# Kernel tuning notes

Hardware: AMD Instinct MI355X
Metric: run time of the kernel (lower is better)

## Reference

```python
import jax, jax.numpy as jnp
import numpy as np

B, S, E = 2, 2048, 5120
HQ, HKV, HD = 32, 8, 128          # q heads, kv heads, head_dim (hard-coded 128 in source)
DQ, DKV = HQ * HD, HKV * HD       # 4096, 1024
ROPE_THETA = 1.0e9
NEG = -1e30


def setup_inputs() -> dict:
    key = jax.random.key(0)
    k0, k1, k2, k3, k4 = jax.random.split(key, 5)
    x = jax.random.normal(k0, (B, S, E), jnp.float32)
    wq = jax.random.normal(k1, (DQ, E), jnp.float32) * 0.02
    wk = jax.random.normal(k2, (DKV, E), jnp.float32) * 0.02
    wv = jax.random.normal(k3, (DKV, E), jnp.float32) * 0.02
    wo = jax.random.normal(k4, (E, DQ), jnp.float32) * 0.02
    # rotary frequencies: complex freqs_cis[s, HD//2] = exp(i * s * theta^{-2j/HD})
    inv_freq = 1.0 / (ROPE_THETA ** (jnp.arange(0, HD, 2, dtype=jnp.float32) / HD))  # [64]
    ang = jnp.arange(S, dtype=jnp.float32)[:, None] * inv_freq[None, :]              # [S, 64]
    return {
        "x": x,
        "freqs_cos": jnp.cos(ang),
        "freqs_sin": jnp.sin(ang),
        "wq": wq, "wk": wk, "wv": wv, "wo": wo,
    }


def _apply_rope(t, cos, sin):
    # t: [b, s, h, HD//2, 2] viewed as complex pairs; cos/sin: [1, s, 1, HD//2]
    tr, ti = t[..., 0], t[..., 1]
    out = jnp.stack([tr * cos - ti * sin, tr * sin + ti * cos], axis=-1)
    b, s, h = t.shape[0], t.shape[1], t.shape[2]
    return out.reshape(b, s, h, HD)


def reference(x, freqs_cos, freqs_sin, wq, wk, wv, wo):
    b, s, _ = x.shape
    q = (x @ wq.T).reshape(b, s, HQ, HD // 2, 2)
    k = (x @ wk.T).reshape(b, s, HKV, HD // 2, 2)
    v = (x @ wv.T).reshape(b, s, HKV, HD)
    cos = freqs_cos[:s][None, :, None, :]
    sin = freqs_sin[:s][None, :, None, :]
    q = _apply_rope(q, cos, sin)                       # [b, s, HQ, HD]
    k = _apply_rope(k, cos, sin)                       # [b, s, HKV, HD]
    # GQA repeat_kv (repeat_interleave along head dim)
    k = jnp.repeat(k, HQ // HKV, axis=2)               # [b, s, HQ, HD]
    v = jnp.repeat(v, HQ // HKV, axis=2)
    q = q.transpose(0, 2, 1, 3)                        # [b, HQ, s, HD]
    k = k.transpose(0, 2, 1, 3)
    v = v.transpose(0, 2, 1, 3)
    scale = 1.0 / np.sqrt(HD).astype(np.float32)
    scores = jnp.einsum('bhqd,bhkd->bhqk', q, k) * scale
    causal = jnp.tril(jnp.ones((s, s), dtype=bool))
    scores = jnp.where(causal[None, None], scores, NEG)
    attn = jax.nn.softmax(scores, axis=-1)
    out = jnp.einsum('bhqk,bhkd->bhqd', attn, v)       # [b, HQ, s, HD]
    out = out.transpose(0, 2, 1, 3).reshape(b, s, DQ)
    return out @ wo.T                                  # [b, s, E]
```

## Files before the change

kernel.cpp:

```cpp
#include <hip/hip_runtime.h>


typedef unsigned short u16;
typedef __bf16 bf16x8 __attribute__((ext_vector_type(8)));
typedef __bf16 bf16x4 __attribute__((ext_vector_type(4)));
typedef float f32x4 __attribute__((ext_vector_type(4)));

__device__ __forceinline__ u16 f2bf(float f) {
  unsigned u = __builtin_bit_cast(unsigned, f);
  u += 0x7fff + ((u >> 16) & 1);
  return (u16)(u >> 16);
}
__device__ __forceinline__ float bf2f(u16 h) {
  unsigned u = ((unsigned)h) << 16;
  return __builtin_bit_cast(float, u);
}

__device__ __forceinline__ float exp2_hw(float x) {
#if __has_builtin(__builtin_amdgcn_exp2f)
  return __builtin_amdgcn_exp2f(x);
#else
  return __expf(x * 0.6931471805599453f);
#endif
}

__device__ __forceinline__ void gload_lds16(const u16* g, u16* lds) {
  __builtin_amdgcn_global_load_lds(
      (const __attribute__((address_space(1))) void*)g,
      (__attribute__((address_space(3))) void*)lds, 16, 0, 0);
}

__device__ __forceinline__ f32x4 mfma16(bf16x8 a, bf16x8 b, f32x4 c) {
  return __builtin_amdgcn_mfma_f32_16x16x32_bf16(a, b, c, 0, 0, 0);
}

#define VMW(N) asm volatile("s_waitcnt vmcnt(" #N ")" ::: "memory")
#define BAR()  __builtin_amdgcn_s_barrier()

__global__ __launch_bounds__(256) void cvt_kernel(const float4* __restrict__ in,
                                                  uint2* __restrict__ out, int n4) {
  int i = blockIdx.x * blockDim.x + threadIdx.x;
  if (i >= n4) return;
  float4 v = in[i];
  unsigned lo = (unsigned)f2bf(v.x) | ((unsigned)f2bf(v.y) << 16);
  unsigned hi = (unsigned)f2bf(v.z) | ((unsigned)f2bf(v.w) << 16);
  out[i] = make_uint2(lo, hi);
}

__global__ __launch_bounds__(256) void rope_kernel(u16* __restrict__ t,
                                                   const float* __restrict__ fcos,
                                                   const float* __restrict__ fsin,
                                                   int hsh, float scale, int total) {
  int idx = blockIdx.x * blockDim.x + threadIdx.x;
  if (idx >= total) return;
  int j = idx & 63;
  int s = (idx >> (6 + hsh)) & 2047;
  float c = fcos[s * 64 + j], sn = fsin[s * 64 + j];
  unsigned* p = (unsigned*)(t + (size_t)idx * 2);
  unsigned v = *p;
  float tr = bf2f((u16)(v & 0xffffu)), ti = bf2f((u16)(v >> 16));
  float orr = (tr * c - ti * sn) * scale;
  float oi  = (tr * sn + ti * c) * scale;
  *p = (unsigned)f2bf(orr) | ((unsigned)f2bf(oi) << 16);
}

template <int MODE>
__global__ __launch_bounds__(256) void gemm_bt(const u16* __restrict__ A,
                                               const u16* __restrict__ B,
                                               void* __restrict__ Cout,
                                               int M, int N, int K) {
  __shared__ u16 As[8192];
  __shared__ u16 Bs[8192];
  const int tid = threadIdx.x;
  const int lane = tid & 63, wave = tid >> 6;
  const int wm = wave >> 1, wn = wave & 1;
  int gx = gridDim.x, nwg = gx * gridDim.y;
  int lin = blockIdx.y * gx + blockIdx.x;
  if ((nwg & 7) == 0) lin = (lin & 7) * (nwg >> 3) + (lin >> 3);
  const int m0 = (lin / gx) * 128, n0 = (lin % gx) * 128;
  const int lc = lane & 15, lg = lane >> 4;

  f32x4 acc[4][4] = {};
  const int sr = tid >> 3, sc = tid & 7;

  for (int kt = 0; kt < K; kt += 64) {
    __syncthreads();
#pragma unroll
    for (int q = 0; q < 4; ++q) {
      int r = q * 32 + sr;
      int cc = sc ^ (r & 7);
      gload_lds16(A + (size_t)(m0 + r) * K + kt + cc * 8, &As[q * 2048 + tid * 8]);
      gload_lds16(B + (size_t)(n0 + r) * K + kt + cc * 8, &Bs[q * 2048 + tid * 8]);
    }
    __syncthreads();
#pragma unroll
    for (int ks = 0; ks < 2; ++ks) {
      bf16x8 af[4], bfr[4];
#pragma unroll
      for (int m = 0; m < 4; ++m) {
        int r = wm * 64 + m * 16 + lc;
        int gc = ks * 4 + lg;
        af[m] = *(const bf16x8*)&As[r * 64 + ((gc ^ (r & 7)) * 8)];
      }
#pragma unroll
      for (int n = 0; n < 4; ++n) {
        int r = wn * 64 + n * 16 + lc;
        int gc = ks * 4 + lg;
        bfr[n] = *(const bf16x8*)&Bs[r * 64 + ((gc ^ (r & 7)) * 8)];
      }
#pragma unroll
      for (int m = 0; m < 4; ++m)
#pragma unroll
        for (int n = 0; n < 4; ++n)
          acc[m][n] = mfma16(af[m], bfr[n], acc[m][n]);
    }
  }

#pragma unroll
  for (int m = 0; m < 4; ++m) {
#pragma unroll
    for (int n = 0; n < 4; ++n) {
#pragma unroll
      for (int i = 0; i < 4; ++i) {
        int gm = m0 + wm * 64 + m * 16 + lg * 4 + i;
        int gn = n0 + wn * 64 + n * 16 + lc;
        float v = acc[m][n][i];
        if (MODE == 0) {
          ((u16*)Cout)[(size_t)gm * N + gn] = f2bf(v);
        } else {
          size_t addr = ((size_t)((gm >> 11) * 8 + (gn >> 7)) * 128 + (gn & 127)) * 2048 +
                        (gm & 2047);
          ((u16*)Cout)[addr] = f2bf(v);
        }
      }
    }
  }
}

template <int OUT_F32>
__global__ __launch_bounds__(512, 2) void gemm256(const u16* __restrict__ A,
                                                  const u16* __restrict__ B,
                                                  void* __restrict__ Cout,
                                                  int M, int N, int K) {
  __shared__ u16 lds[2][2][2][8192];
  const int tid = threadIdx.x, lane = tid & 63, wave = tid >> 6;
  const int wm = wave >> 2;
  const int wn = wave & 3;
  const int lc = lane & 15, lg = lane >> 4;
  const int srow = lane >> 3;
  const int cc8  = ((lane & 7) ^ srow) * 8;
  const int bh   = wn >> 1;
  const int sb   = wm * 2 + (wn & 1);

  int gx = gridDim.x, nwg = gx * gridDim.y;
  int lin = blockIdx.y * gx + blockIdx.x;
  if ((nwg & 7) == 0) lin = (lin & 7) * (nwg >> 3) + (lin >> 3);
  const int m0 = (lin / gx) * 256, n0 = (lin % gx) * 256;

  auto stA = [&](int buf, int kcol, int rowBase) {
    int rb = rowBase + wn * 8;
    gload_lds16(A + (size_t)(m0 + wm * 128 + rb + srow) * K + kcol + cc8,
                &lds[buf][0][wm][rb * 64 + lane * 8]);
  };
  auto stB = [&](int buf, int kcol, int rowBase) {
    int rb = rowBase + sb * 8;
    gload_lds16(B + (size_t)(n0 + bh * 128 + rb + srow) * K + kcol + cc8,
                &lds[buf][1][bh][rb * 64 + lane * 8]);
  };
  auto stageAll = [&](int buf, int kcol) {
    stA(buf, kcol, 0);  stB(buf, kcol, 0);
    stA(buf, kcol, 32); stB(buf, kcol, 32);
    stA(buf, kcol, 64); stB(buf, kcol, 64);
    stA(buf, kcol, 96); stB(buf, kcol, 96);
  };

  f32x4 acc[8][4] = {};
  bf16x8 af[4][2], bfv[4][2];

  stageAll(0, 0);

  const int nk = K >> 6;
  for (int t = 0; t < nk; ++t) {
    const int cur = t & 1;
    if (t + 1 < nk) {
      stageAll(cur ^ 1, (t + 1) << 6);
      VMW(8);
    } else {
      VMW(0);
    }
    BAR();
    const u16* Ah = &lds[cur][0][wm][0];
    const u16* Bh = &lds[cur][1][bh][0];

#pragma unroll
    for (int m = 0; m < 4; ++m)
#pragma unroll
      for (int kg = 0; kg < 2; ++kg) {
        int r = m * 16 + lc;
        af[m][kg] = *(const bf16x8*)&Ah[r * 64 + (((kg * 4 + lg) ^ (r & 7)) * 8)];
      }
#pragma unroll
    for (int n = 0; n < 2; ++n)
#pragma unroll
      for (int kg = 0; kg < 2; ++kg) {
        int r = (wn & 1) * 64 + n * 16 + lc;
        bfv[n][kg] = *(const bf16x8*)&Bh[r * 64 + (((kg * 4 + lg) ^ (r & 7)) * 8)];
      }
    __builtin_amdgcn_s_setprio(1);
#pragma unroll
    for (int m = 0; m < 4; ++m)
#pragma unroll
      for (int n = 0; n < 2; ++n)
#pragma unroll
        for (int kg = 0; kg < 2; ++kg)
          acc[m][n] = mfma16(af[m][kg], bfv[n][kg], acc[m][n]);
    __builtin_amdgcn_s_setprio(0);

#pragma unroll
    for (int n = 2; n < 4; ++n)
#pragma unroll
      for (int kg = 0; kg < 2; ++kg) {
        int r = (wn & 1) * 64 + n * 16 + lc;
        bfv[n][kg] = *(const bf16x8*)&Bh[r * 64 + (((kg * 4 + lg) ^ (r & 7)) * 8)];
      }
    __builtin_amdgcn_s_setprio(1);
#pragma unroll
    for (int m = 0; m < 4; ++m)
#pragma unroll
      for (int n = 2; n < 4; ++n)
#pragma unroll
        for (int kg = 0; kg < 2; ++kg)
          acc[m][n] = mfma16(af[m][kg], bfv[n][kg], acc[m][n]);
    __builtin_amdgcn_s_setprio(0);

#pragma unroll
    for (int m = 0; m < 4; ++m)
#pragma unroll
      for (int kg = 0; kg < 2; ++kg) {
        int r = 64 + m * 16 + lc;
        af[m][kg] = *(const bf16x8*)&Ah[r * 64 + (((kg * 4 + lg) ^ (r & 7)) * 8)];
      }
    __builtin_amdgcn_s_setprio(1);
#pragma unroll
    for (int m = 0; m < 4; ++m)
#pragma unroll
      for (int n = 0; n < 4; ++n)
#pragma unroll
        for (int kg = 0; kg < 2; ++kg)
          acc[4 + m][n] = mfma16(af[m][kg], bfv[n][kg], acc[4 + m][n]);
    __builtin_amdgcn_s_setprio(0);

    BAR();
  }

#pragma unroll
  for (int m = 0; m < 8; ++m) {
#pragma unroll
    for (int n = 0; n < 4; ++n) {
#pragma unroll
      for (int i = 0; i < 4; ++i) {
        int gm = m0 + wm * 128 + m * 16 + lg * 4 + i;
        int gn = n0 + wn * 64 + n * 16 + lc;
        float v = acc[m][n][i];
        if (OUT_F32) ((float*)Cout)[(size_t)gm * N + gn] = v;
        else         ((u16*)Cout)[(size_t)gm * N + gn] = f2bf(v);
      }
    }
  }
}

__global__ __launch_bounds__(256) void attn_kernel(const u16* __restrict__ Q,
                                                   const u16* __restrict__ Kg,
                                                   const u16* __restrict__ VT,
                                                   u16* __restrict__ AO) {
  __shared__ u16 Ks[2][8192];
  __shared__ u16 Vs[2][8192];
  __shared__ u16 P_lds[4][16 * 72];
  const int tid = threadIdx.x, lane = tid & 63, w = tid >> 6;
  const int qt = (int)gridDim.x - 1 - (int)blockIdx.x;
  const int h = blockIdx.y, b = blockIdx.z;
  const int hkv = h >> 2;
  const int q0 = qt * 64;
  const int lc = lane & 15, lg = lane >> 4;

  bf16x8 qf[4];
  {
    const size_t qrow = ((size_t)(b * 2048 + q0 + w * 16 + lc) * 32 + h) * 128;
#pragma unroll
    for (int ks = 0; ks < 4; ++ks) qf[ks] = *(const bf16x8*)&Q[qrow + ks * 32 + lg * 8];
  }

  f32x4 o[8] = {};
  f32x4 lsum = {0.f, 0.f, 0.f, 0.f};

  const int nsteps = qt + 1;
  const size_t kpanel = ((size_t)b * 2048 * 8 + hkv) * 128;
  const size_t vpanel = ((size_t)(b * 8 + hkv) * 128) * 2048;

  auto stage = [&](int buf, int step) {
    const int kv0 = step * 64;
#pragma unroll
    for (int p = 0; p < 4; ++p) {
      int r = p * 16 + (tid >> 4);
      int cc = (tid & 15) ^ (r & 15);
      gload_lds16(Kg + kpanel + (size_t)(kv0 + r) * 1024 + cc * 8,
                  &Ks[buf][p * 2048 + tid * 8]);
    }
#pragma unroll
    for (int p = 0; p < 4; ++p) {
      int r = p * 32 + (tid >> 3);
      int cc = (tid & 7) ^ (r & 7);
      gload_lds16(VT + vpanel + (size_t)r * 2048 + kv0 + cc * 8,
                  &Vs[buf][p * 2048 + tid * 8]);
    }
  };

  stage(0, 0);

  for (int step = 0; step < nsteps; ++step) {
    const int kv0 = step * 64;
    __syncthreads();
    if (step + 1 < nsteps) stage((step + 1) & 1, step + 1);
    const u16* kb = Ks[step & 1];
    const u16* vb = Vs[step & 1];

    f32x4 s[4];
#pragma unroll
    for (int nf = 0; nf < 4; ++nf) s[nf] = f32x4{0.f, 0.f, 0.f, 0.f};
    __builtin_amdgcn_s_setprio(1);
#pragma unroll
    for (int ks = 0; ks < 4; ++ks) {
#pragma unroll
      for (int nf = 0; nf < 4; ++nf) {
        int r = nf * 16 + lc;
        int gc = ks * 4 + lg;
        bf16x8 kf = *(const bf16x8*)&kb[r * 128 + ((gc ^ (r & 15)) * 8)];
        s[nf] = mfma16(kf, qf[ks], s[nf]);
      }
    }
    __builtin_amdgcn_s_setprio(0);

    if (step == qt) {
      int q = q0 + w * 16 + lc;
#pragma unroll
      for (int nf = 0; nf < 4; ++nf) {
#pragma unroll
        for (int i = 0; i < 4; ++i) {
          int kv = kv0 + nf * 16 + lg * 4 + i;
          if (kv > q) s[nf][i] = -1e30f;
        }
      }
    }

#pragma unroll
    for (int nf = 0; nf < 4; ++nf) {
#pragma unroll
      for (int i = 0; i < 4; ++i) s[nf][i] = exp2_hw(s[nf][i]);
      lsum += s[nf];
      bf16x4 pw = {(__bf16)s[nf][0], (__bf16)s[nf][1], (__bf16)s[nf][2], (__bf16)s[nf][3]};
      *(bf16x4*)&P_lds[w][lc * 72 + nf * 16 + lg * 4] = pw;
    }
    asm volatile("s_waitcnt lgkmcnt(0)" ::: "memory");
    __builtin_amdgcn_sched_barrier(0);

    bf16x8 pa[2];
#pragma unroll
    for (int ksv = 0; ksv < 2; ++ksv)
      pa[ksv] = *(const bf16x8*)&P_lds[w][lc * 72 + ksv * 32 + lg * 8];

    __builtin_amdgcn_s_setprio(1);
#pragma unroll
    for (int nfd = 0; nfd < 8; ++nfd) {
#pragma unroll
      for (int ksv = 0; ksv < 2; ++ksv) {
        int r = nfd * 16 + lc;
        int gc = ksv * 4 + lg;
        bf16x8 vf = *(const bf16x8*)&vb[r * 64 + ((gc ^ (r & 7)) * 8)];
        o[nfd] = mfma16(pa[ksv], vf, o[nfd]);
      }
    }
    __builtin_amdgcn_s_setprio(0);
  }

  float t = lsum[0] + lsum[1] + lsum[2] + lsum[3];
  t += __shfl_xor(t, 16, 64);
  t += __shfl_xor(t, 32, 64);
  float linv[4];
#pragma unroll
  for (int i = 0; i < 4; ++i) linv[i] = 1.0f / __shfl(t, lg * 4 + i, 64);

#pragma unroll
  for (int nfd = 0; nfd < 8; ++nfd)
#pragma unroll
    for (int i = 0; i < 4; ++i) {
      int row = q0 + w * 16 + lg * 4 + i;
      AO[((size_t)(b * 2048 + row) * 32 + h) * 128 + nfd * 16 + lc] =
          f2bf(o[nfd][i] * linv[i]);
    }
}

extern "C" void kernel_launch(void* const* d_in, const int* in_sizes, int n_in,
                              void* d_out, int out_size, void* d_ws, size_t ws_size,
                              hipStream_t stream) {
  const float* x    = (const float*)d_in[0];
  const float* fcos = (const float*)d_in[1];
  const float* fsin = (const float*)d_in[2];
  const float* wq   = (const float*)d_in[3];
  const float* wk   = (const float*)d_in[4];
  const float* wv   = (const float*)d_in[5];
  const float* wo   = (const float*)d_in[6];
  float* out = (float*)d_out;

  char* ws = (char*)d_ws;
  u16* xb  = (u16*)(ws + 0);
  u16* wqb = (u16*)(ws + 41943040ull);
  u16* wkb = (u16*)(ws + 83886080ull);
  u16* wvb = (u16*)(ws + 94371840ull);
  u16* Qb  = (u16*)(ws + 104857600ull);
  u16* Kb  = (u16*)(ws + 138412032ull);
  u16* VTb = (u16*)(ws + 146800640ull);
  u16* AOb = xb;
  u16* wob = wqb;

  auto cvt = [&](const float* src, u16* dst, int nelem) {
    int n4 = nelem / 4;
    cvt_kernel<<<dim3((n4 + 255) / 256), dim3(256), 0, stream>>>((const float4*)src,
                                                                 (uint2*)dst, n4);
  };
  cvt(x, xb, 2 * 2048 * 5120);
  cvt(wq, wqb, 4096 * 5120);
  cvt(wk, wkb, 1024 * 5120);
  cvt(wv, wvb, 1024 * 5120);

  dim3 blk(256);
  gemm256<0><<<dim3(16, 16), dim3(512), 0, stream>>>(xb, wqb, Qb, 4096, 4096, 5120);
  gemm_bt<0><<<dim3(8, 32), blk, 0, stream>>>(xb, wkb, Kb, 4096, 1024, 5120);
  gemm_bt<2><<<dim3(8, 32), blk, 0, stream>>>(xb, wvb, VTb, 4096, 1024, 5120);

  cvt(wo, wob, 5120 * 4096);

  const float qscale = 0.12751743558818574f;
  rope_kernel<<<dim3(8388608 / 256), blk, 0, stream>>>(Qb, fcos, fsin, 5, qscale, 8388608);
  rope_kernel<<<dim3(2097152 / 256), blk, 0, stream>>>(Kb, fcos, fsin, 3, 1.0f, 2097152);

  attn_kernel<<<dim3(32, 32, 2), blk, 0, stream>>>(Qb, Kb, VTb, AOb);

  gemm256<1><<<dim3(20, 16), dim3(512), 0, stream>>>(AOb, wob, out, 4096, 5120, 4096);
}
```

Measured before the change: 854.2 us.

## Interleave quarter-tile global-to-LDS loads with MFMA phases in gemm256

Restructures the 256x256 GEMM main loop so the A and B halves of the next tiles are staged in four separate pieces, each issued between MFMA sub-phases with barriers and partial vmcnt waits. Prefetch reaches up to two k-steps ahead, and a dummy LDS buffer absorbs out-of-range loads so the instruction count stays uniform. The aim is to overlap memory traffic with compute more finely than one bulk stage per iteration. In exchange it adds many barriers per iteration and extra LDS use, which may lower occupancy.

```diff
diff --git a/kernel.cpp b/kernel.cpp
--- a/kernel.cpp
+++ b/kernel.cpp
@@ -143,69 +143,76 @@
                                                   void* __restrict__ Cout,
                                                   int M, int N, int K) {
   __shared__ u16 lds[2][2][2][8192];
+  __shared__ u16 dummy[4096];
   const int tid = threadIdx.x, lane = tid & 63, wave = tid >> 6;
   const int wm = wave >> 2;
   const int wn = wave & 3;
   const int lc = lane & 15, lg = lane >> 4;
-  const int srow = lane >> 3;
-  const int cc8  = ((lane & 7) ^ srow) * 8;
-  const int bh   = wn >> 1;
-  const int sb   = wm * 2 + (wn & 1);
+  const int bh = wn >> 1;
+  const int bs64 = (wn & 1) * 64;
+  const int str = tid >> 3, ssc = tid & 7;
 
   int gx = gridDim.x, nwg = gx * gridDim.y;
   int lin = blockIdx.y * gx + blockIdx.x;
   if ((nwg & 7) == 0) lin = (lin & 7) * (nwg >> 3) + (lin >> 3);
   const int m0 = (lin / gx) * 256, n0 = (lin % gx) * 256;
 
-  auto stA = [&](int buf, int kcol, int rowBase) {
-    int rb = rowBase + wn * 8;
-    gload_lds16(A + (size_t)(m0 + wm * 128 + rb + srow) * K + kcol + cc8,
-                &lds[buf][0][wm][rb * 64 + lane * 8]);
+  auto stageA = [&](int buf, int kcol, int r0, bool real) {
+    int r = r0 + str, cc = ssc ^ (r & 7);
+    const u16* s = A + (size_t)(m0 + r) * K + kcol + cc * 8;
+    u16* d0 = real ? &lds[buf][0][0][r0 * 64] : dummy;
+    u16* d1 = real ? &lds[buf][0][1][r0 * 64] : dummy;
+    gload_lds16(s, d0 + tid * 8);
+    gload_lds16(s + (size_t)128 * K, d1 + tid * 8);
   };
-  auto stB = [&](int buf, int kcol, int rowBase) {
-    int rb = rowBase + sb * 8;
-    gload_lds16(B + (size_t)(n0 + bh * 128 + rb + srow) * K + kcol + cc8,
-                &lds[buf][1][bh][rb * 64 + lane * 8]);
-  };
-  auto stageAll = [&](int buf, int kcol) {
-    stA(buf, kcol, 0);  stB(buf, kcol, 0);
-    stA(buf, kcol, 32); stB(buf, kcol, 32);
-    stA(buf, kcol, 64); stB(buf, kcol, 64);
-    stA(buf, kcol, 96); stB(buf, kcol, 96);
+  auto stageB = [&](int buf, int kcol, int half, bool real) {
+    int r = str, cc = ssc ^ (r & 7);
+    int r2 = 64 + str, cc2 = ssc ^ (r2 & 7);
+    const u16* s = B + (size_t)(n0 + half * 128) * K + kcol;
+    u16* d0 = real ? &lds[buf][1][half][0] : dummy;
+    u16* d1 = real ? &lds[buf][1][half][4096] : dummy;
+    gload_lds16(s + (size_t)r * K + cc * 8, d0 + tid * 8);
+    gload_lds16(s + (size_t)r2 * K + cc2 * 8, d1 + tid * 8);
   };
 
   f32x4 acc[8][4] = {};
   bf16x8 af[4][2], bfv[4][2];
 
-  stageAll(0, 0);
-
   const int nk = K >> 6;
+  stageB(0, 0, 0, true);
+  stageA(0, 0, 0, true);
+  stageB(0, 0, 1, true);
+  stageA(0, 0, 64, true);
+  stageB(1, 64, 0, true);
+  stageA(1, 64, 0, true);
+  VMW(6);
+  BAR();
+
   for (int t = 0; t < nk; ++t) {
-    const int cur = t & 1;
-    if (t + 1 < nk) {
-      stageAll(cur ^ 1, (t + 1) << 6);
-      VMW(8);
-    } else {
-      VMW(0);
-    }
-    BAR();
-    const u16* Ah = &lds[cur][0][wm][0];
-    const u16* Bh = &lds[cur][1][bh][0];
+    const int c = t & 1;
+    const int t1 = t + 1, t2 = t + 2;
+    const int kc1 = (t1 < nk ? t1 : nk - 1) << 6;
+    const int kc2 = (t2 < nk ? t2 : nk - 1) << 6;
+    const bool h1 = t1 < nk, h2 = t2 < nk;
+    const u16* Ab = &lds[c][0][wm][0];
+    const u16* Bb = &lds[c][1][bh][0];
 
 #pragma unroll
     for (int m = 0; m < 4; ++m)
 #pragma unroll
       for (int kg = 0; kg < 2; ++kg) {
         int r = m * 16 + lc;
-        af[m][kg] = *(const bf16x8*)&Ah[r * 64 + (((kg * 4 + lg) ^ (r & 7)) * 8)];
+        af[m][kg] = *(const bf16x8*)&Ab[r * 64 + (((kg * 4 + lg) ^ (r & 7)) * 8)];
       }
 #pragma unroll
     for (int n = 0; n < 2; ++n)
 #pragma unroll
       for (int kg = 0; kg < 2; ++kg) {
-        int r = (wn & 1) * 64 + n * 16 + lc;
-        bfv[n][kg] = *(const bf16x8*)&Bh[r * 64 + (((kg * 4 + lg) ^ (r & 7)) * 8)];
-      }
+        int r = bs64 + n * 16 + lc;
+        bfv[n][kg] = *(const bf16x8*)&Bb[r * 64 + (((kg * 4 + lg) ^ (r & 7)) * 8)];
+      }
+    stageB(t1 & 1, kc1, 1, h1);
+    BAR();
     __builtin_amdgcn_s_setprio(1);
 #pragma unroll
     for (int m = 0; m < 4; ++m)
@@ -215,14 +222,18 @@
         for (int kg = 0; kg < 2; ++kg)
           acc[m][n] = mfma16(af[m][kg], bfv[n][kg], acc[m][n]);
     __builtin_amdgcn_s_setprio(0);
+    BAR();
 
 #pragma unroll
     for (int n = 2; n < 4; ++n)
 #pragma unroll
       for (int kg = 0; kg < 2; ++kg) {
-        int r = (wn & 1) * 64 + n * 16 + lc;
-        bfv[n][kg] = *(const bf16x8*)&Bh[r * 64 + (((kg * 4 + lg) ^ (r & 7)) * 8)];
-      }
+        int r = bs64 + n * 16 + lc;
+        bfv[n][kg] = *(const bf16x8*)&Bb[r * 64 + (((kg * 4 + lg) ^ (r & 7)) * 8)];
+      }
+    stageA(t1 & 1, kc1, 64, h1);
+    VMW(6);
+    BAR();
     __builtin_amdgcn_s_setprio(1);
 #pragma unroll
     for (int m = 0; m < 4; ++m)
@@ -232,24 +243,40 @@
         for (int kg = 0; kg < 2; ++kg)
           acc[m][n] = mfma16(af[m][kg], bfv[n][kg], acc[m][n]);
     __builtin_amdgcn_s_setprio(0);
+    BAR();
 
 #pragma unroll
     for (int m = 0; m < 4; ++m)
 #pragma unroll
       for (int kg = 0; kg < 2; ++kg) {
         int r = 64 + m * 16 + lc;
-        af[m][kg] = *(const bf16x8*)&Ah[r * 64 + (((kg * 4 + lg) ^ (r & 7)) * 8)];
-      }
-    __builtin_amdgcn_s_setprio(1);
-#pragma unroll
-    for (int m = 0; m < 4; ++m)
-#pragma unroll
-      for (int n = 0; n < 4; ++n)
+        af[m][kg] = *(const bf16x8*)&Ab[r * 64 + (((kg * 4 + lg) ^ (r & 7)) * 8)];
+      }
+    stageB(t2 & 1, kc2, 0, h2);
+    BAR();
+    __builtin_amdgcn_s_setprio(1);
+#pragma unroll
+    for (int m = 0; m < 4; ++m)
+#pragma unroll
+      for (int n = 0; n < 2; ++n)
 #pragma unroll
         for (int kg = 0; kg < 2; ++kg)
           acc[4 + m][n] = mfma16(af[m][kg], bfv[n][kg], acc[4 + m][n]);
     __builtin_amdgcn_s_setprio(0);
-
+    BAR();
+
+    stageA(t2 & 1, kc2, 0, h2);
+    VMW(6);
+    BAR();
+    __builtin_amdgcn_s_setprio(1);
+#pragma unroll
+    for (int m = 0; m < 4; ++m)
+#pragma unroll
+      for (int n = 2; n < 4; ++n)
+#pragma unroll
+        for (int kg = 0; kg < 2; ++kg)
+          acc[4 + m][n] = mfma16(af[m][kg], bfv[n][kg], acc[4 + m][n]);
+    __builtin_amdgcn_s_setprio(0);
     BAR();
   }
 
```

After: 828.8 us. 1.03x faster.
